# Performance work log

Measured on AMD Instinct MI355X. Metric: run time of the kernel, lower is better.

The kernel has to match this reference:

```python
import jax, jax.numpy as jnp
import numpy as np

B, T, VALUE_DIM = 128, 2048, 128
ATTN_DIM, RNN_DIM, NUM_CLASSES = 10, 64, 4000
HS = (RNN_DIM + VALUE_DIM) // 2  # 96
STEPS = 32


def setup_inputs() -> dict:
    key = jax.random.key(0)
    ks = jax.random.split(key, 30)
    def p(k, shape, scale=0.08):
        return jax.random.normal(k, shape, dtype=jnp.float32) * scale
    return {
        "encoder_outputs": jax.random.normal(ks[0], (B, T, VALUE_DIM), dtype=jnp.float32),
        # 2-layer unidirectional GRU (torch layout: W_ih (3H, in), W_hh (3H, H))
        "rnn_w_ih0": p(ks[1], (3 * RNN_DIM, ATTN_DIM)),
        "rnn_w_hh0": p(ks[2], (3 * RNN_DIM, RNN_DIM)),
        "rnn_b_ih0": p(ks[3], (3 * RNN_DIM,)),
        "rnn_b_hh0": p(ks[4], (3 * RNN_DIM,)),
        "rnn_w_ih1": p(ks[5], (3 * RNN_DIM, RNN_DIM)),
        "rnn_w_hh1": p(ks[6], (3 * RNN_DIM, RNN_DIM)),
        "rnn_b_ih1": p(ks[7], (3 * RNN_DIM,)),
        "rnn_b_hh1": p(ks[8], (3 * RNN_DIM,)),
        # location-aware attention
        "attn_conv_w": p(ks[9], (ATTN_DIM, 1, 3)),   # Conv1d(1, A, k=3, pad=1)
        "attn_conv_b": p(ks[10], (ATTN_DIM,)),
        "attn_wq": p(ks[11], (ATTN_DIM, RNN_DIM)),
        "attn_bq": p(ks[12], (ATTN_DIM,)),
        "attn_wv": p(ks[13], (ATTN_DIM, VALUE_DIM)),
        "attn_bias": p(ks[14], (ATTN_DIM,)),
        "attn_score_w": p(ks[15], (ATTN_DIM,)),
        "attn_score_b": p(ks[16], (1,)),
        # classifier MLP: 192 -> 96 -> 48 -> num_classes
        "fc_w1": p(ks[17], (HS, 2 * HS)),
        "fc_b1": p(ks[18], (HS,)),
        "fc_w2": p(ks[19], (HS // 2, HS)),
        "fc_b2": p(ks[20], (HS // 2,)),
        "fc_w3": p(ks[21], (NUM_CLASSES, HS // 2)),
        "fc_b3": p(ks[22], (NUM_CLASSES,)),
        "targets_max_length": STEPS,
    }


def _gru_cell(x, h, w_ih, w_hh, b_ih, b_hh):
    gi = x @ w_ih.T + b_ih
    gh = h @ w_hh.T + b_hh
    i_r, i_z, i_n = jnp.split(gi, 3, axis=-1)
    h_r, h_z, h_n = jnp.split(gh, 3, axis=-1)
    r = jax.nn.sigmoid(i_r + h_r)
    z = jax.nn.sigmoid(i_z + h_z)
    n = jnp.tanh(i_n + r * h_n)
    return (1.0 - z) * n + z * h


def reference(encoder_outputs, rnn_w_ih0, rnn_w_hh0, rnn_b_ih0, rnn_b_hh0,
              rnn_w_ih1, rnn_w_hh1, rnn_b_ih1, rnn_b_hh1,
              attn_conv_w, attn_conv_b, attn_wq, attn_bq, attn_wv, attn_bias,
              attn_score_w, attn_score_b,
              fc_w1, fc_b1, fc_w2, fc_b2, fc_w3, fc_b3, targets_max_length):
    Bn, Tn, _ = encoder_outputs.shape
    H = rnn_w_hh0.shape[1]
    A = rnn_w_ih0.shape[1]
    # value projection is step-invariant: hoist out of the decode loop
    v_proj = jnp.einsum('btv,av->bta', encoder_outputs, attn_wv)  # (B,T,A)
    x0 = jnp.zeros((Bn, A), dtype=encoder_outputs.dtype)  # per-step RNN input

    def step(carry, _):
        h0, h1, last_attn = carry
        h0 = _gru_cell(x0, h0, rnn_w_ih0, rnn_w_hh0, rnn_b_ih0, rnn_b_hh0)
        h1 = _gru_cell(h0, h1, rnn_w_ih1, rnn_w_hh1, rnn_b_ih1, rnn_b_hh1)
        # location feature: Conv1d over previous attention weights
        loc = jax.lax.conv_general_dilated(
            last_attn[:, None, :], attn_conv_w, (1,), 'SAME',
            dimension_numbers=('NCH', 'OIH', 'NCH'))  # (B,A,T)
        loc = jnp.transpose(loc, (0, 2, 1)) + attn_conv_b  # (B,T,A)
        e = jnp.tanh((h1 @ attn_wq.T + attn_bq)[:, None, :] + v_proj + loc + attn_bias)
        score = e @ attn_score_w + attn_score_b  # (B,T)
        attn = jax.nn.softmax(score, axis=-1)
        context = jnp.einsum('bt,btv->bv', attn, encoder_outputs)  # (B,value_dim)
        hcat = jnp.concatenate([h1, context], axis=-1)  # (B, 2*HS)
        y = jax.nn.relu(hcat @ fc_w1.T + fc_b1)
        y = jax.nn.relu(y @ fc_w2.T + fc_b2)
        logits = y @ fc_w3.T + fc_b3
        logp = jax.nn.log_softmax(logits, axis=-1)
        return (h0, h1, attn), (logp, attn)

    init = (jnp.zeros((Bn, H), dtype=encoder_outputs.dtype),
            jnp.zeros((Bn, H), dtype=encoder_outputs.dtype),
            jnp.zeros((Bn, Tn), dtype=encoder_outputs.dtype))
    _, (logps, attns) = jax.lax.scan(step, init, None, length=int(targets_max_length))
    # (steps, B, ...) -> (B, steps, ...)
    return jnp.transpose(logps, (1, 0, 2)), jnp.transpose(attns, (1, 0, 2))
```

## Files before the change

kernel.cpp:

```cpp
#include <hip/hip_runtime.h>
#include <cstddef>

#define Bn 128
#define Tn 2048
#define Vn 128
#define An 10
#define Hn 64
#define NCn 4000
#define STEPSn 32
#define SCH 16
#define TCH 512
#define PREP_ROWS 64
#define NB_PREP ((Bn * Tn) / PREP_ROWS)

__device__ __forceinline__ float waveReduceSum(float v) {
    #pragma unroll
    for (int off = 32; off > 0; off >>= 1) v += __shfl_xor(v, off, 64);
    return v;
}

__device__ __forceinline__ unsigned short f2bf(float f) {
    unsigned u = __float_as_uint(f);
    u += 0x7fffu + ((u >> 16) & 1u);
    return (unsigned short)(u >> 16);
}

__global__ __launch_bounds__(640) void gru_kernel(
    const float* __restrict__ w_hh0, const float* __restrict__ b_ih0, const float* __restrict__ b_hh0,
    const float* __restrict__ w_ih1, const float* __restrict__ w_hh1,
    const float* __restrict__ b_ih1, const float* __restrict__ b_hh1,
    const float* __restrict__ wq, const float* __restrict__ bq, const float* __restrict__ abias,
    float* __restrict__ h1_all, float* __restrict__ qq_all)
{
    const int tid = threadIdx.x;
    __shared__ float h0[Hn], h1[Hn], g0[192], g1i[192], g1h[192];

    float w[64];
    float bias = 0.f;
    int role = -1, row = 0;
    const float* wsrc = nullptr;
    if (tid < 192)      { role = 0; row = tid;       wsrc = w_hh0 + row * 64; bias = b_hh0[row]; }
    else if (tid < 384) { role = 1; row = tid - 192; wsrc = w_hh1 + row * 64; bias = b_hh1[row]; }
    else if (tid < 576) { role = 2; row = tid - 384; wsrc = w_ih1 + row * 64; bias = b_ih1[row]; }
    else if (tid < 586) { role = 3; row = tid - 576; wsrc = wq    + row * 64; bias = bq[row] + abias[row]; }
    if (wsrc) {
        const float4* w4 = (const float4*)wsrc;
        #pragma unroll
        for (int k = 0; k < 16; ++k) {
            float4 v = w4[k];
            w[4*k] = v.x; w[4*k+1] = v.y; w[4*k+2] = v.z; w[4*k+3] = v.w;
        }
    }
    float bi0r = 0.f, bi0z = 0.f, bi0n = 0.f;
    if (tid < Hn) {
        bi0r = b_ih0[tid]; bi0z = b_ih0[64 + tid]; bi0n = b_ih0[128 + tid];
        h0[tid] = 0.f; h1[tid] = 0.f;
    }
    __syncthreads();

    #define DOT64(dst, src) { \
        float a0 = 0.f, a1 = 0.f, a2 = 0.f, a3 = 0.f; \
        _Pragma("unroll") \
        for (int k = 0; k < 64; k += 4) { \
            a0 = fmaf(w[k],   src[k],   a0); a1 = fmaf(w[k+1], src[k+1], a1); \
            a2 = fmaf(w[k+2], src[k+2], a2); a3 = fmaf(w[k+3], src[k+3], a3); \
        } \
        dst = bias + ((a0 + a1) + (a2 + a3)); \
    }

    for (int s = 0; s < STEPSn; ++s) {
        if (role == 0)      { DOT64(g0[row],  h0); }
        else if (role == 1) { DOT64(g1h[row], h1); }
        else if (role == 3 && s > 0) { float q; DOT64(q, h1); qq_all[(s - 1) * 16 + row] = q; }
        __syncthreads();
        if (tid < Hn) {
            float r = 1.f / (1.f + __expf(-(bi0r + g0[tid])));
            float z = 1.f / (1.f + __expf(-(bi0z + g0[64 + tid])));
            float n = tanhf(bi0n + r * g0[128 + tid]);
            h0[tid] = (1.f - z) * n + z * h0[tid];
        }
        __syncthreads();
        if (role == 2) { DOT64(g1i[row], h0); }
        __syncthreads();
        if (tid < Hn) {
            float r = 1.f / (1.f + __expf(-(g1i[tid]      + g1h[tid])));
            float z = 1.f / (1.f + __expf(-(g1i[64 + tid] + g1h[64 + tid])));
            float n = tanhf(g1i[128 + tid] + r * g1h[128 + tid]);
            float hn = (1.f - z) * n + z * h1[tid];
            h1[tid] = hn;
            h1_all[s * Hn + tid] = hn;
        }
        __syncthreads();
    }
    if (role == 3) { float q; DOT64(q, h1); qq_all[31 * 16 + row] = q; }
    #undef DOT64
}

__global__ __launch_bounds__(256) void prep_kernel(
    const float* __restrict__ enc, const float* __restrict__ wv,
    unsigned short* __restrict__ enc16, unsigned short* __restrict__ vp16)
{
    const int tid = threadIdx.x;
    __shared__ float sh[PREP_ROWS][132];
    __shared__ float wvsT[128][12];

    const size_t row0 = (size_t)blockIdx.x * PREP_ROWS;
    for (int i = tid; i < 128 * An; i += 256) {
        int k = i / An, a = i - k * An;
        wvsT[k][a] = wv[a * 128 + k];
    }
    for (int i = tid; i < PREP_ROWS * 32; i += 256) {
        int r = i >> 5, kq = i & 31;
        float4 v = ((const float4*)(enc + (row0 + r) * 128))[kq];
        *(float4*)&sh[r][kq * 4] = v;
        ushort4 o;
        o.x = f2bf(v.x); o.y = f2bf(v.y); o.z = f2bf(v.z); o.w = f2bf(v.w);
        ((ushort4*)(enc16 + (row0 + r) * 128))[kq] = o;
    }
    __syncthreads();

    for (int i = tid; i < PREP_ROWS * An; i += 256) {
        int r = i / An, a = i - r * An;
        float acc = 0.f;
        #pragma unroll
        for (int k = 0; k < 128; k += 4) {
            float4 e = *(const float4*)&sh[r][k];
            acc = fmaf(e.x, wvsT[k][a],   acc);
            acc = fmaf(e.y, wvsT[k+1][a], acc);
            acc = fmaf(e.z, wvsT[k+2][a], acc);
            acc = fmaf(e.w, wvsT[k+3][a], acc);
        }
        vp16[(row0 + r) * An + a] = f2bf(acc);
    }
}

__global__ __launch_bounds__(1024, 4) void score_chain_kernel(
    const unsigned short* __restrict__ vp16, const float* __restrict__ qq_all,
    const float* __restrict__ conv_w, const float* __restrict__ conv_b,
    const float* __restrict__ score_w, const float* __restrict__ score_b,
    float* __restrict__ psum_all, float* __restrict__ out_attn)
{
    const int b = blockIdx.x;
    const int tid = threadIdx.x;
    __shared__ float la[2][Tn + 2];
    __shared__ float red[17];
    __shared__ float qsh[STEPSn * 16];

    for (int i = tid; i < 2 * (Tn + 2); i += 1024) ((float*)la)[i] = 0.f;
    if (tid < STEPSn * 16) qsh[tid] = qq_all[tid];
    __syncthreads();

    float cw0[An], cw1[An], cw2[An], qb[An], nsw2[An];
    float sb0 = score_b[0];
    #pragma unroll
    for (int a = 0; a < An; ++a) {
        cw0[a] = conv_w[3*a]; cw1[a] = conv_w[3*a+1]; cw2[a] = conv_w[3*a+2];
        qb[a] = conv_b[a];
        float s = score_w[a];
        sb0 += s;
        nsw2[a] = -2.f * s;
    }

    float va[2][An];
    {
        const unsigned* vpb = (const unsigned*)(vp16 + (size_t)b * Tn * An);
        #pragma unroll
        for (int half = 0; half < 2; ++half) {
            const unsigned* vpt = vpb + (size_t)(tid + half * 1024) * 5;
            #pragma unroll
            for (int k = 0; k < 5; ++k) {
                unsigned u = vpt[k];
                va[half][2*k]   = __uint_as_float(u << 16);
                va[half][2*k+1] = __uint_as_float(u & 0xffff0000u);
            }
        }
    }

    float* oa = out_attn + (size_t)b * STEPSn * Tn;
    int cur = 0;
    float inv = 1.f;

    for (int s = 0; s < STEPSn; ++s) {
        float qc[An], c0[An], c1[An], c2[An];
        #pragma unroll
        for (int a = 0; a < An; ++a) {
            qc[a] = qsh[s * 16 + a] + qb[a];
            c0[a] = cw0[a] * inv;
            c1[a] = cw1[a] * inv;
            c2[a] = cw2[a] * inv;
        }

        const int nxt = cur ^ 1;
        float pv[2];
        float psum_loc = 0.f;
        #pragma unroll
        for (int half = 0; half < 2; ++half) {
            int t = tid + half * 1024;
            float l = la[cur][t];
            float m = la[cur][t + 1];
            float r = la[cur][t + 2];
            float ssum = sb0;
            #pragma unroll
            for (int a = 0; a < An; ++a) {
                float arg = fmaf(c0[a], l, fmaf(c1[a], m, fmaf(c2[a], r, qc[a] + va[half][a])));
                float e = __expf(arg + arg);
                ssum = fmaf(nsw2[a], __builtin_amdgcn_rcpf(e + 1.f), ssum);
            }
            float p = __expf(ssum);
            la[nxt][t + 1] = p;
            pv[half] = p;
            psum_loc += p;
        }
        float wsum = waveReduceSum(psum_loc);
        if ((tid & 63) == 0) red[tid >> 6] = wsum;
        __syncthreads();
        if (tid < 16) {
            float v = red[tid];
            #pragma unroll
            for (int m2 = 8; m2 > 0; m2 >>= 1) v += __shfl_xor(v, m2, 64);
            if (tid == 0) { red[16] = v; psum_all[b * STEPSn + s] = v; }
        }
        __syncthreads();
        float tot = red[16];
        inv = 1.f / tot;
        oa[(size_t)s * Tn + tid]        = pv[0] * inv;
        oa[(size_t)s * Tn + tid + 1024] = pv[1] * inv;
        cur = nxt;
    }
}

__global__ __launch_bounds__(256) void ctx_kernel(
    const unsigned short* __restrict__ enc16,
    const float* __restrict__ out_attn, float* __restrict__ pctx)
{
    const int bid = blockIdx.x;
    const int sc = bid & 1, tc = (bid >> 1) & 3, b = bid >> 3;
    const int t0 = tc * TCH, s0 = sc * SCH;
    const int tid = threadIdx.x;

    __shared__ float shbuf[SCH * TCH];

    for (int i = tid; i < SCH * TCH; i += 256) {
        int si = i >> 9, ti = i & (TCH - 1);
        shbuf[si * TCH + ti] = out_attn[((size_t)b * STEPSn + s0 + si) * Tn + t0 + ti];
    }
    __syncthreads();

    const int lane = tid & 63, w = tid >> 6;
    float accx[SCH], accy[SCH];
    #pragma unroll
    for (int si = 0; si < SCH; ++si) { accx[si] = 0.f; accy[si] = 0.f; }

    for (int t4 = w * 4; t4 < TCH; t4 += 16) {
        float ex[4], ey[4];
        #pragma unroll
        for (int u = 0; u < 4; ++u) {
            unsigned uu = ((const unsigned*)enc16)[((size_t)b * Tn + t0 + t4 + u) * 64 + lane];
            ex[u] = __uint_as_float(uu << 16);
            ey[u] = __uint_as_float(uu & 0xffff0000u);
        }
        #pragma unroll
        for (int si = 0; si < SCH; ++si) {
            float4 p4 = *(const float4*)&shbuf[si * TCH + t4];
            accx[si] = fmaf(p4.x, ex[0], accx[si]); accy[si] = fmaf(p4.x, ey[0], accy[si]);
            accx[si] = fmaf(p4.y, ex[1], accx[si]); accy[si] = fmaf(p4.y, ey[1], accy[si]);
            accx[si] = fmaf(p4.z, ex[2], accx[si]); accy[si] = fmaf(p4.z, ey[2], accy[si]);
            accx[si] = fmaf(p4.w, ex[3], accx[si]); accy[si] = fmaf(p4.w, ey[3], accy[si]);
        }
    }
    __syncthreads();
    #pragma unroll
    for (int si = 0; si < SCH; ++si) {
        shbuf[((w * SCH) + si) * Vn + 2 * lane]     = accx[si];
        shbuf[((w * SCH) + si) * Vn + 2 * lane + 1] = accy[si];
    }
    __syncthreads();
    for (int o = tid; o < SCH * Vn; o += 256) {
        int si = o >> 7, v = o & (Vn - 1);
        float s2 = shbuf[si * Vn + v] + shbuf[(SCH + si) * Vn + v]
                 + shbuf[(2 * SCH + si) * Vn + v] + shbuf[(3 * SCH + si) * Vn + v];
        pctx[(((size_t)b * STEPSn + s0 + si) * 4 + tc) * Vn + v] = s2;
    }
}

__global__ __launch_bounds__(128) void mlp_kernel(
    const float* __restrict__ h1_all, const float* __restrict__ pctx,
    const float* __restrict__ fc_w1, const float* __restrict__ fc_b1,
    const float* __restrict__ fc_w2, const float* __restrict__ fc_b2,
    float* __restrict__ y2_all)
{
    const int bs = blockIdx.x;
    const int s = bs & 31;
    const int tid = threadIdx.x;
    __shared__ float hcat[192], y1[96];
    if (tid < Hn) hcat[tid] = h1_all[s * Hn + tid];
    {
        const float* pc = pctx + (size_t)bs * 4 * Vn;
        hcat[Hn + tid] = pc[tid] + pc[Vn + tid] + pc[2 * Vn + tid] + pc[3 * Vn + tid];
    }
    __syncthreads();
    if (tid < 96) {
        float acc = fc_b1[tid];
        const float4* wr = (const float4*)(fc_w1 + tid * 192);
        #pragma unroll
        for (int k = 0; k < 48; ++k) {
            float4 w = wr[k];
            acc += w.x*hcat[4*k] + w.y*hcat[4*k+1] + w.z*hcat[4*k+2] + w.w*hcat[4*k+3];
        }
        y1[tid] = fmaxf(acc, 0.f);
    }
    __syncthreads();
    if (tid < 48) {
        float acc = fc_b2[tid];
        const float4* wr = (const float4*)(fc_w2 + tid * 96);
        #pragma unroll
        for (int k = 0; k < 24; ++k) {
            float4 w = wr[k];
            acc += w.x*y1[4*k] + w.y*y1[4*k+1] + w.z*y1[4*k+2] + w.w*y1[4*k+3];
        }
        y2_all[(size_t)bs * 48 + tid] = fmaxf(acc, 0.f);
    }
}

__global__ __launch_bounds__(256) void logit_kernel(
    const float* __restrict__ y2_all, const float* __restrict__ fc_w3,
    const float* __restrict__ fc_b3,
    float* __restrict__ esum_part, float* __restrict__ out_logp)
{
    const int gx = blockIdx.x;
    const int gy = blockIdx.y;
    const int tid = threadIdx.x;
    const int lane = tid & 63;
    const int wid = __builtin_amdgcn_readfirstlane(tid >> 6);
    const int c = gx * 64 + lane;
    const bool cv = (c < NCn);

    float4 w[12];
    float bias = 0.f;
    if (cv) {
        const float4* wr = (const float4*)(fc_w3 + (size_t)c * 48);
        #pragma unroll
        for (int j = 0; j < 12; ++j) w[j] = wr[j];
        bias = fc_b3[c];
    } else {
        #pragma unroll
        for (int j = 0; j < 12; ++j) w[j] = make_float4(0.f, 0.f, 0.f, 0.f);
    }

    const int r0 = gy * 16 + wid * 4;
    #pragma unroll
    for (int rr = 0; rr < 4; ++rr) {
        const int row = r0 + rr;
        const float* y2r = y2_all + (size_t)row * 48;
        float a0 = bias, a1 = 0.f, a2 = 0.f, a3 = 0.f;
        #pragma unroll
        for (int j = 0; j < 12; ++j) {
            float4 ww = w[j];
            a0 = fmaf(y2r[4*j],     ww.x, a0);
            a1 = fmaf(y2r[4*j + 1], ww.y, a1);
            a2 = fmaf(y2r[4*j + 2], ww.z, a2);
            a3 = fmaf(y2r[4*j + 3], ww.w, a3);
        }
        float lg = (a0 + a1) + (a2 + a3);
        float ex = 0.f;
        if (cv) {
            out_logp[(size_t)row * NCn + c] = lg;
            ex = __expf(lg);
        }
        ex = waveReduceSum(ex);
        if (lane == 0) esum_part[(size_t)row * 64 + gx] = ex;
    }
}

__global__ __launch_bounds__(256) void esum_reduce_kernel(const float* __restrict__ esum_part,
                                                          float* __restrict__ lse_all) {
    int row = blockIdx.x * 256 + threadIdx.x;
    if (row >= Bn * STEPSn) return;
    const float* p = esum_part + (size_t)row * 64;
    float s = 0.f;
    #pragma unroll
    for (int i = 0; i < 63; ++i) s += p[i];
    lse_all[row] = logf(s);
}

__global__ __launch_bounds__(256) void fixlogp_kernel(float* __restrict__ out_logp,
                                                      const float* __restrict__ lse_all) {
    size_t idx4 = (size_t)blockIdx.x * 256 + threadIdx.x;
    int pair = (int)((idx4 * 4) / NCn);
    float lse = lse_all[pair];
    float4 v = ((float4*)out_logp)[idx4];
    v.x -= lse; v.y -= lse; v.z -= lse; v.w -= lse;
    ((float4*)out_logp)[idx4] = v;
}

extern "C" void kernel_launch(void* const* d_in, const int* in_sizes, int n_in,
                              void* d_out, int out_size, void* d_ws, size_t ws_size,
                              hipStream_t stream) {
    const float* enc    = (const float*)d_in[0];
    const float* w_hh0  = (const float*)d_in[2];
    const float* b_ih0  = (const float*)d_in[3];
    const float* b_hh0  = (const float*)d_in[4];
    const float* w_ih1  = (const float*)d_in[5];
    const float* w_hh1  = (const float*)d_in[6];
    const float* b_ih1  = (const float*)d_in[7];
    const float* b_hh1  = (const float*)d_in[8];
    const float* conv_w = (const float*)d_in[9];
    const float* conv_b = (const float*)d_in[10];
    const float* wq     = (const float*)d_in[11];
    const float* bq     = (const float*)d_in[12];
    const float* wv     = (const float*)d_in[13];
    const float* abias  = (const float*)d_in[14];
    const float* sw     = (const float*)d_in[15];
    const float* sb     = (const float*)d_in[16];
    const float* fc_w1  = (const float*)d_in[17];
    const float* fc_b1  = (const float*)d_in[18];
    const float* fc_w2  = (const float*)d_in[19];
    const float* fc_b2  = (const float*)d_in[20];
    const float* fc_w3  = (const float*)d_in[21];
    const float* fc_b3  = (const float*)d_in[22];

    size_t off = 0;
    float* wsf = (float*)d_ws;
    float* psum_all  = wsf + off; off += (size_t)Bn * STEPSn;
    float* lse_all   = wsf + off; off += (size_t)Bn * STEPSn;
    float* h1_all    = wsf + off; off += (size_t)STEPSn * Hn;
    float* qq_all    = wsf + off; off += (size_t)STEPSn * 16;
    float* y2_all    = wsf + off; off += (size_t)Bn * STEPSn * 48;
    float* esum_part = wsf + off; off += (size_t)Bn * STEPSn * 64;
    float* pctx      = wsf + off; off += (size_t)Bn * STEPSn * 4 * Vn;
    unsigned short* vp16  = (unsigned short*)(wsf + off); off += (size_t)Bn * Tn * An / 2;
    unsigned short* enc16 = (unsigned short*)(wsf + off); off += (size_t)Bn * Tn * Vn / 2;

    float* out_logp = (float*)d_out;
    float* out_attn = out_logp + (size_t)Bn * STEPSn * NCn;

    gru_kernel<<<1, 640, 0, stream>>>(w_hh0, b_ih0, b_hh0, w_ih1, w_hh1, b_ih1, b_hh1,
                                      wq, bq, abias, h1_all, qq_all);

    prep_kernel<<<NB_PREP, 256, 0, stream>>>(enc, wv, enc16, vp16);

    score_chain_kernel<<<Bn, 1024, 0, stream>>>(vp16, qq_all, conv_w, conv_b, sw, sb,
                                                psum_all, out_attn);

    ctx_kernel<<<Bn * 4 * 2, 256, 0, stream>>>(enc16, out_attn, pctx);

    mlp_kernel<<<Bn * STEPSn, 128, 0, stream>>>(h1_all, pctx, fc_w1, fc_b1, fc_w2, fc_b2, y2_all);

    logit_kernel<<<dim3(63, 256), 256, 0, stream>>>(y2_all, fc_w3, fc_b3, esum_part, out_logp);

    esum_reduce_kernel<<<(Bn * STEPSn + 255) / 256, 256, 0, stream>>>(esum_part, lse_all);

    fixlogp_kernel<<<(unsigned)((size_t)Bn * STEPSn * NCn / 4 / 256), 256, 0, stream>>>(out_logp, lse_all);
}
```

Before: 359.1 us.

## Fuse GRU into prep kernel, simplify score reduction, restructure ctx kernel

The single-block GRU recurrence now runs as an extra block of the prep kernel. The prep kernel grows to 640 threads, one per (row, attention-dim) output, which removes a launch and lets the serial GRU overlap with the encoder conversion. In the score chain, the second barrier per step is dropped: partial sums are double-buffered by step parity and every thread sums the 16 wave partials itself. The ctx kernel now covers all 32 steps per block, reads attention weights straight from global memory instead of staging them in shared memory, and launches half as many blocks. This doubles the per-thread accumulator count, which raises register pressure and lowers parallelism in ctx.

```diff
diff --git a/kernel.cpp b/kernel.cpp
--- a/kernel.cpp
+++ b/kernel.cpp
@@ -8,7 +8,7 @@
 #define Hn 64
 #define NCn 4000
 #define STEPSn 32
-#define SCH 16
+#define SCH 32
 #define TCH 512
 #define PREP_ROWS 64
 #define NB_PREP ((Bn * Tn) / PREP_ROWS)
@@ -25,91 +25,89 @@
     return (unsigned short)(u >> 16);
 }
 
-__global__ __launch_bounds__(640) void gru_kernel(
+__global__ __launch_bounds__(640) void prep_kernel(
+    const float* __restrict__ enc, const float* __restrict__ wv,
     const float* __restrict__ w_hh0, const float* __restrict__ b_ih0, const float* __restrict__ b_hh0,
     const float* __restrict__ w_ih1, const float* __restrict__ w_hh1,
     const float* __restrict__ b_ih1, const float* __restrict__ b_hh1,
     const float* __restrict__ wq, const float* __restrict__ bq, const float* __restrict__ abias,
+    unsigned short* __restrict__ enc16, unsigned short* __restrict__ vp16,
     float* __restrict__ h1_all, float* __restrict__ qq_all)
-{
-    const int tid = threadIdx.x;
-    __shared__ float h0[Hn], h1[Hn], g0[192], g1i[192], g1h[192];
-
-    float w[64];
-    float bias = 0.f;
-    int role = -1, row = 0;
-    const float* wsrc = nullptr;
-    if (tid < 192)      { role = 0; row = tid;       wsrc = w_hh0 + row * 64; bias = b_hh0[row]; }
-    else if (tid < 384) { role = 1; row = tid - 192; wsrc = w_hh1 + row * 64; bias = b_hh1[row]; }
-    else if (tid < 576) { role = 2; row = tid - 384; wsrc = w_ih1 + row * 64; bias = b_ih1[row]; }
-    else if (tid < 586) { role = 3; row = tid - 576; wsrc = wq    + row * 64; bias = bq[row] + abias[row]; }
-    if (wsrc) {
-        const float4* w4 = (const float4*)wsrc;
-        #pragma unroll
-        for (int k = 0; k < 16; ++k) {
-            float4 v = w4[k];
-            w[4*k] = v.x; w[4*k+1] = v.y; w[4*k+2] = v.z; w[4*k+3] = v.w;
-        }
-    }
-    float bi0r = 0.f, bi0z = 0.f, bi0n = 0.f;
-    if (tid < Hn) {
-        bi0r = b_ih0[tid]; bi0z = b_ih0[64 + tid]; bi0n = b_ih0[128 + tid];
-        h0[tid] = 0.f; h1[tid] = 0.f;
-    }
-    __syncthreads();
-
-    #define DOT64(dst, src) { \
-        float a0 = 0.f, a1 = 0.f, a2 = 0.f, a3 = 0.f; \
-        _Pragma("unroll") \
-        for (int k = 0; k < 64; k += 4) { \
-            a0 = fmaf(w[k],   src[k],   a0); a1 = fmaf(w[k+1], src[k+1], a1); \
-            a2 = fmaf(w[k+2], src[k+2], a2); a3 = fmaf(w[k+3], src[k+3], a3); \
-        } \
-        dst = bias + ((a0 + a1) + (a2 + a3)); \
-    }
-
-    for (int s = 0; s < STEPSn; ++s) {
-        if (role == 0)      { DOT64(g0[row],  h0); }
-        else if (role == 1) { DOT64(g1h[row], h1); }
-        else if (role == 3 && s > 0) { float q; DOT64(q, h1); qq_all[(s - 1) * 16 + row] = q; }
-        __syncthreads();
-        if (tid < Hn) {
-            float r = 1.f / (1.f + __expf(-(bi0r + g0[tid])));
-            float z = 1.f / (1.f + __expf(-(bi0z + g0[64 + tid])));
-            float n = tanhf(bi0n + r * g0[128 + tid]);
-            h0[tid] = (1.f - z) * n + z * h0[tid];
-        }
-        __syncthreads();
-        if (role == 2) { DOT64(g1i[row], h0); }
-        __syncthreads();
-        if (tid < Hn) {
-            float r = 1.f / (1.f + __expf(-(g1i[tid]      + g1h[tid])));
-            float z = 1.f / (1.f + __expf(-(g1i[64 + tid] + g1h[64 + tid])));
-            float n = tanhf(g1i[128 + tid] + r * g1h[128 + tid]);
-            float hn = (1.f - z) * n + z * h1[tid];
-            h1[tid] = hn;
-            h1_all[s * Hn + tid] = hn;
-        }
-        __syncthreads();
-    }
-    if (role == 3) { float q; DOT64(q, h1); qq_all[31 * 16 + row] = q; }
-    #undef DOT64
-}
-
-__global__ __launch_bounds__(256) void prep_kernel(
-    const float* __restrict__ enc, const float* __restrict__ wv,
-    unsigned short* __restrict__ enc16, unsigned short* __restrict__ vp16)
 {
     const int tid = threadIdx.x;
     __shared__ float sh[PREP_ROWS][132];
     __shared__ float wvsT[128][12];
+    __shared__ float h0[Hn], h1[Hn], g0[192], g1i[192], g1h[192];
+
+    if (blockIdx.x == NB_PREP) {
+        float w[64];
+        float bias = 0.f;
+        int role = -1, row = 0;
+        const float* wsrc = nullptr;
+        if (tid < 192)      { role = 0; row = tid;       wsrc = w_hh0 + row * 64; bias = b_hh0[row]; }
+        else if (tid < 384) { role = 1; row = tid - 192; wsrc = w_hh1 + row * 64; bias = b_hh1[row]; }
+        else if (tid < 576) { role = 2; row = tid - 384; wsrc = w_ih1 + row * 64; bias = b_ih1[row]; }
+        else if (tid < 586) { role = 3; row = tid - 576; wsrc = wq    + row * 64; bias = bq[row] + abias[row]; }
+        if (wsrc) {
+            const float4* w4 = (const float4*)wsrc;
+            #pragma unroll
+            for (int k = 0; k < 16; ++k) {
+                float4 v = w4[k];
+                w[4*k] = v.x; w[4*k+1] = v.y; w[4*k+2] = v.z; w[4*k+3] = v.w;
+            }
+        }
+        float bi0r = 0.f, bi0z = 0.f, bi0n = 0.f;
+        if (tid < Hn) {
+            bi0r = b_ih0[tid]; bi0z = b_ih0[64 + tid]; bi0n = b_ih0[128 + tid];
+            h0[tid] = 0.f; h1[tid] = 0.f;
+        }
+        __syncthreads();
+
+        #define DOT64(dst, src) { \
+            float a0 = 0.f, a1 = 0.f, a2 = 0.f, a3 = 0.f; \
+            _Pragma("unroll") \
+            for (int k = 0; k < 64; k += 4) { \
+                a0 = fmaf(w[k],   src[k],   a0); a1 = fmaf(w[k+1], src[k+1], a1); \
+                a2 = fmaf(w[k+2], src[k+2], a2); a3 = fmaf(w[k+3], src[k+3], a3); \
+            } \
+            dst = bias + ((a0 + a1) + (a2 + a3)); \
+        }
+
+        for (int s = 0; s < STEPSn; ++s) {
+            if (role == 0)      { DOT64(g0[row],  h0); }
+            else if (role == 1) { DOT64(g1h[row], h1); }
+            else if (role == 3 && s > 0) { float q; DOT64(q, h1); qq_all[(s - 1) * 16 + row] = q; }
+            __syncthreads();
+            if (tid < Hn) {
+                float r = 1.f / (1.f + __expf(-(bi0r + g0[tid])));
+                float z = 1.f / (1.f + __expf(-(bi0z + g0[64 + tid])));
+                float n = tanhf(bi0n + r * g0[128 + tid]);
+                h0[tid] = (1.f - z) * n + z * h0[tid];
+            }
+            __syncthreads();
+            if (role == 2) { DOT64(g1i[row], h0); }
+            __syncthreads();
+            if (tid < Hn) {
+                float r = 1.f / (1.f + __expf(-(g1i[tid]      + g1h[tid])));
+                float z = 1.f / (1.f + __expf(-(g1i[64 + tid] + g1h[64 + tid])));
+                float n = tanhf(g1i[128 + tid] + r * g1h[128 + tid]);
+                float hn = (1.f - z) * n + z * h1[tid];
+                h1[tid] = hn;
+                h1_all[s * Hn + tid] = hn;
+            }
+            __syncthreads();
+        }
+        if (role == 3) { float q; DOT64(q, h1); qq_all[31 * 16 + row] = q; }
+        #undef DOT64
+        return;
+    }
 
     const size_t row0 = (size_t)blockIdx.x * PREP_ROWS;
-    for (int i = tid; i < 128 * An; i += 256) {
+    for (int i = tid; i < 128 * An; i += 640) {
         int k = i / An, a = i - k * An;
         wvsT[k][a] = wv[a * 128 + k];
     }
-    for (int i = tid; i < PREP_ROWS * 32; i += 256) {
+    for (int i = tid; i < PREP_ROWS * 32; i += 640) {
         int r = i >> 5, kq = i & 31;
         float4 v = ((const float4*)(enc + (row0 + r) * 128))[kq];
         *(float4*)&sh[r][kq * 4] = v;
@@ -119,8 +117,8 @@
     }
     __syncthreads();
 
-    for (int i = tid; i < PREP_ROWS * An; i += 256) {
-        int r = i / An, a = i - r * An;
+    {
+        int r = tid / An, a = tid - r * An;
         float acc = 0.f;
         #pragma unroll
         for (int k = 0; k < 128; k += 4) {
@@ -143,7 +141,7 @@
     const int b = blockIdx.x;
     const int tid = threadIdx.x;
     __shared__ float la[2][Tn + 2];
-    __shared__ float red[17];
+    __shared__ float red[2][16];
     __shared__ float qsh[STEPSn * 16];
 
     for (int i = tid; i < 2 * (Tn + 2); i += 1024) ((float*)la)[i] = 0.f;
@@ -212,16 +210,12 @@
             psum_loc += p;
         }
         float wsum = waveReduceSum(psum_loc);
-        if ((tid & 63) == 0) red[tid >> 6] = wsum;
+        if ((tid & 63) == 0) red[s & 1][tid >> 6] = wsum;
         __syncthreads();
-        if (tid < 16) {
-            float v = red[tid];
-            #pragma unroll
-            for (int m2 = 8; m2 > 0; m2 >>= 1) v += __shfl_xor(v, m2, 64);
-            if (tid == 0) { red[16] = v; psum_all[b * STEPSn + s] = v; }
-        }
-        __syncthreads();
-        float tot = red[16];
+        float tot = 0.f;
+        #pragma unroll
+        for (int i = 0; i < 16; ++i) tot += red[s & 1][i];
+        if (tid == 0) psum_all[b * STEPSn + s] = tot;
         inv = 1.f / tot;
         oa[(size_t)s * Tn + tid]        = pv[0] * inv;
         oa[(size_t)s * Tn + tid + 1024] = pv[1] * inv;
@@ -234,22 +228,19 @@
     const float* __restrict__ out_attn, float* __restrict__ pctx)
 {
     const int bid = blockIdx.x;
-    const int sc = bid & 1, tc = (bid >> 1) & 3, b = bid >> 3;
-    const int t0 = tc * TCH, s0 = sc * SCH;
+    const int tc = bid & 3, b = bid >> 2;
+    const int t0 = tc * TCH;
     const int tid = threadIdx.x;
-
-    __shared__ float shbuf[SCH * TCH];
-
-    for (int i = tid; i < SCH * TCH; i += 256) {
-        int si = i >> 9, ti = i & (TCH - 1);
-        shbuf[si * TCH + ti] = out_attn[((size_t)b * STEPSn + s0 + si) * Tn + t0 + ti];
-    }
-    __syncthreads();
-
-    const int lane = tid & 63, w = tid >> 6;
+    const int lane = tid & 63;
+    const int w = __builtin_amdgcn_readfirstlane(tid >> 6);
+
+    __shared__ float part[4 * SCH * Vn];
+
     float accx[SCH], accy[SCH];
     #pragma unroll
     for (int si = 0; si < SCH; ++si) { accx[si] = 0.f; accy[si] = 0.f; }
+
+    const float* ab = out_attn + (size_t)b * STEPSn * Tn + t0;
 
     for (int t4 = w * 4; t4 < TCH; t4 += 16) {
         float ex[4], ey[4];
@@ -261,25 +252,24 @@
         }
         #pragma unroll
         for (int si = 0; si < SCH; ++si) {
-            float4 p4 = *(const float4*)&shbuf[si * TCH + t4];
+            float4 p4 = *(const float4*)(ab + (size_t)si * Tn + t4);
             accx[si] = fmaf(p4.x, ex[0], accx[si]); accy[si] = fmaf(p4.x, ey[0], accy[si]);
             accx[si] = fmaf(p4.y, ex[1], accx[si]); accy[si] = fmaf(p4.y, ey[1], accy[si]);
             accx[si] = fmaf(p4.z, ex[2], accx[si]); accy[si] = fmaf(p4.z, ey[2], accy[si]);
             accx[si] = fmaf(p4.w, ex[3], accx[si]); accy[si] = fmaf(p4.w, ey[3], accy[si]);
         }
     }
-    __syncthreads();
     #pragma unroll
     for (int si = 0; si < SCH; ++si) {
-        shbuf[((w * SCH) + si) * Vn + 2 * lane]     = accx[si];
-        shbuf[((w * SCH) + si) * Vn + 2 * lane + 1] = accy[si];
+        part[((w * SCH) + si) * Vn + 2 * lane]     = accx[si];
+        part[((w * SCH) + si) * Vn + 2 * lane + 1] = accy[si];
     }
     __syncthreads();
     for (int o = tid; o < SCH * Vn; o += 256) {
         int si = o >> 7, v = o & (Vn - 1);
-        float s2 = shbuf[si * Vn + v] + shbuf[(SCH + si) * Vn + v]
-                 + shbuf[(2 * SCH + si) * Vn + v] + shbuf[(3 * SCH + si) * Vn + v];
-        pctx[(((size_t)b * STEPSn + s0 + si) * 4 + tc) * Vn + v] = s2;
+        float s2 = part[si * Vn + v] + part[(SCH + si) * Vn + v]
+                 + part[(2 * SCH + si) * Vn + v] + part[(3 * SCH + si) * Vn + v];
+        pctx[(((size_t)b * STEPSn + si) * 4 + tc) * Vn + v] = s2;
     }
 }
 
@@ -434,15 +424,14 @@
     float* out_logp = (float*)d_out;
     float* out_attn = out_logp + (size_t)Bn * STEPSn * NCn;
 
-    gru_kernel<<<1, 640, 0, stream>>>(w_hh0, b_ih0, b_hh0, w_ih1, w_hh1, b_ih1, b_hh1,
-                                      wq, bq, abias, h1_all, qq_all);
-
-    prep_kernel<<<NB_PREP, 256, 0, stream>>>(enc, wv, enc16, vp16);
+    prep_kernel<<<NB_PREP + 1, 640, 0, stream>>>(
+        enc, wv, w_hh0, b_ih0, b_hh0, w_ih1, w_hh1, b_ih1, b_hh1,
+        wq, bq, abias, enc16, vp16, h1_all, qq_all);
 
     score_chain_kernel<<<Bn, 1024, 0, stream>>>(vp16, qq_all, conv_w, conv_b, sw, sb,
                                                 psum_all, out_attn);
 
-    ctx_kernel<<<Bn * 4 * 2, 256, 0, stream>>>(enc16, out_attn, pctx);
+    ctx_kernel<<<Bn * 4, 256, 0, stream>>>(enc16, out_attn, pctx);
 
     mlp_kernel<<<Bn * STEPSn, 128, 0, stream>>>(h1_all, pctx, fc_w1, fc_b1, fc_w2, fc_b2, y2_all);
 
```

New measurement: 414.7 us. +15.5%, slower.
